# Kernel tuning notes

Hardware: AMD Instinct MI355X
Metric: run time of the kernel (lower is better)

## Reference

```python
import jax, jax.numpy as jnp
import numpy as np

B, T, S, D = 16, 64, 256, 512
NEG_INF = -1e9  # finite stand-in for -inf mask fill (identical sparsemax output, autodiff-safe)


def sparsemax(z, axis=-1):
    # sparsemax(z) = clip(z - tau, 0), tau from sorted cumsum threshold
    z = z - jnp.max(z, axis=axis, keepdims=True)
    z_srt = -jnp.sort(-z, axis=axis)                      # descending sort
    z_cum = jnp.cumsum(z_srt, axis=axis) - 1.0
    k = jnp.arange(1, z.shape[axis] + 1, dtype=z.dtype)   # rho = 1..d
    support = (k * z_srt) > z_cum
    supp_size = jnp.sum(support, axis=axis, keepdims=True)
    tau = jnp.take_along_axis(z_cum, supp_size - 1, axis=axis) / supp_size.astype(z.dtype)
    return jnp.clip(z - tau, 0.0)


def setup_inputs() -> dict:
    key = jax.random.key(0)
    ks = jax.random.split(key, 9)
    init = lambda k, shape: (jax.random.normal(k, shape, jnp.float32) * 0.05)
    return {
        "source": jax.random.normal(ks[0], (B, T, D), jnp.float32),
        "memory_bank": jax.random.normal(ks[1], (B, S, D), jnp.float32),
        "memory_mask": jax.random.randint(ks[2], (B, S), 0, 2).astype(jnp.int32),
        "W_q": init(ks[3], (D, D)),   # linear_query weight
        "b_q": init(ks[4], (D,)),     # linear_query bias
        "W_c": init(ks[5], (D, D)),   # linear_context weight (no bias)
        "v": init(ks[6], (D,)),       # v projection (dim -> 1)
        "W_out": init(ks[7], (D, 2 * D)),  # linear_out weight
        "b_out": init(ks[8], (D,)),        # linear_out bias (mlp path has bias)
    }


def reference(source, memory_bank, memory_mask, W_q, b_q, W_c, v, W_out, b_out):
    # MLP (Bahdanau) score: v^T tanh(W_q q + U_c h)
    wq = jnp.einsum('btd,ed->bte', source, W_q) + b_q        # (B,T,D)
    uh = jnp.einsum('bsd,ed->bse', memory_bank, W_c)         # (B,S,D)
    wquh = jnp.tanh(wq[:, :, None, :] + uh[:, None, :, :])   # (B,T,S,D) big intermediate
    align = jnp.einsum('btsd,d->bts', wquh, v)               # (B,T,S)
    align = jnp.where(memory_mask[:, None, :].astype(bool), align, NEG_INF)
    align_vectors = sparsemax(align, axis=-1)                # (B,T,S)
    c = jnp.einsum('bts,bsd->btd', align_vectors, memory_bank)
    concat_c = jnp.concatenate([c, source], axis=-1)         # (B,T,2D)
    attn_h = jnp.einsum('btf,df->btd', concat_c, W_out) + b_out  # no tanh on mlp path
    return attn_h.transpose(1, 0, 2), align_vectors.transpose(1, 0, 2)
```

## Files before the change

### kernel.cpp

```cpp
#include <hip/hip_runtime.h>
#include <hip/hip_bf16.h>

#define BB 16
#define TT 64
#define SS 256
#define DD 512

typedef __bf16 bf16x8 __attribute__((ext_vector_type(8)));
typedef float f32x4 __attribute__((ext_vector_type(4)));

__device__ __forceinline__ ushort f2b(float x) {
    __hip_bfloat16 h = __float2bfloat16(x);
    return __builtin_bit_cast(ushort, h);
}
__device__ __forceinline__ float b2f(ushort u) {
    unsigned int x = (unsigned int)u << 16;
    return __builtin_bit_cast(float, x);
}
__device__ __forceinline__ void gload16(const ushort* g, ushort* l) {
    __builtin_amdgcn_global_load_lds(
        (const __attribute__((address_space(1))) unsigned int*)g,
        (__attribute__((address_space(3))) unsigned int*)l, 16, 0, 0);
}

#define S_SRC (BB * TT * DD)
#define S_MB  (BB * SS * DD)
#define S_WQ  (DD * DD)
#define S_WC  (DD * DD)
#define S_WO  (DD * 2 * DD)

__global__ __launch_bounds__(256) void cast_all(
    const float* __restrict__ src, const float* __restrict__ mb,
    const float* __restrict__ wq, const float* __restrict__ wc,
    const float* __restrict__ wo,
    ushort* __restrict__ src_b, ushort* __restrict__ mb_b,
    ushort* __restrict__ wq_b, ushort* __restrict__ wc_b,
    ushort* __restrict__ wo_b) {
    int g = blockIdx.x * 256 + threadIdx.x;
    const int G0 = S_SRC / 4, G1 = S_MB / 4, G2 = S_WQ / 4, G3 = S_WC / 4;
    const float* in;
    ushort* out;
    int local;
    if (g < G0) { in = src; out = src_b; local = g; }
    else if (g < G0 + G1) { in = mb; out = mb_b; local = g - G0; }
    else if (g < G0 + G1 + G2) { in = wq; out = wq_b; local = g - G0 - G1; }
    else if (g < G0 + G1 + G2 + G3) { in = wc; out = wc_b; local = g - G0 - G1 - G2; }
    else { in = wo; out = wo_b; local = g - G0 - G1 - G2 - G3; }
    float4 x = *(const float4*)(in + (size_t)local * 4);
    ushort4 y = {f2b(x.x), f2b(x.y), f2b(x.z), f2b(x.w)};
    *(ushort4*)(out + (size_t)local * 4) = y;
}

__global__ __launch_bounds__(256) void mega_gemm(
    const ushort* __restrict__ src_b, const ushort* __restrict__ mb_b,
    const ushort* __restrict__ wq_b, const ushort* __restrict__ wc_b,
    const ushort* __restrict__ wo_b,
    const float* __restrict__ b_q, const float* __restrict__ b_out,
    float* __restrict__ Ewq, float* __restrict__ Y,
    ushort* __restrict__ Eu, ushort* __restrict__ M2) {
    __shared__ ushort Asm[64 * 64];
    __shared__ ushort Bsm[64 * 64];
    const int id = blockIdx.x;
    const ushort* Ab;
    const ushort* Bb;
    const float* bias = nullptr;
    void* Cp;
    int ldb, N, m0, n0;
    bool exp2x, obf16, hasb;
    size_t coff = 0;
    if (id < 256) {
        const bool isY = id >= 128;
        const int l = id & 127;
        m0 = (l >> 3) * 64; n0 = (l & 7) * 64;
        Ab = src_b;
        Bb = isY ? (wo_b + DD) : wq_b;
        ldb = isY ? 2 * DD : DD;
        bias = isY ? b_out : b_q;
        hasb = true; exp2x = !isY; obf16 = false; N = DD;
        Cp = isY ? (void*)Y : (void*)Ewq;
    } else if (id < 768) {
        const int l = id - 256;
        const int bz = l >> 5, tl = l & 31;
        m0 = (tl >> 3) * 64; n0 = (tl & 7) * 64;
        Ab = mb_b + (size_t)bz * SS * DD;
        Bb = wc_b;
        ldb = DD;
        hasb = false; exp2x = true; obf16 = true; N = DD;
        Cp = (void*)Eu; coff = (size_t)bz * SS * DD;
    } else {
        const int l = id - 768;
        const int bz = l >> 5, tl = l & 31;
        m0 = (tl >> 3) * 64; n0 = (tl & 7) * 64;
        Ab = mb_b + (size_t)bz * SS * DD;
        Bb = wo_b;
        ldb = 2 * DD;
        hasb = false; exp2x = false; obf16 = true; N = DD;
        Cp = (void*)M2; coff = (size_t)bz * SS * DD;
    }

    const int tid = threadIdx.x;
    const int lane = tid & 63;
    const int wave = tid >> 6;
    const int wm = wave & 1, wn = wave >> 1;

    const int rl = lane >> 3;
    const int csw = (lane & 7) ^ rl;
    const ushort* Ag0 = Ab + (size_t)(m0 + wave * 16 + rl) * DD + csw * 8;
    const ushort* Ag1 = Ag0 + (size_t)8 * DD;
    const ushort* Bg0 = Bb + (size_t)(n0 + wave * 16 + rl) * ldb + csw * 8;
    const ushort* Bg1 = Bg0 + (size_t)8 * ldb;
    ushort* Al0 = &Asm[(wave * 16) * 64];
    ushort* Al1 = &Asm[(wave * 16 + 8) * 64];
    ushort* Bl0 = &Bsm[(wave * 16) * 64];
    ushort* Bl1 = &Bsm[(wave * 16 + 8) * 64];

    const int l15 = lane & 15, quad = lane >> 4;
    const int xr = l15 & 7;
    const int arow0 = (wm * 32 + l15) * 64, arow1 = arow0 + 16 * 64;
    const int brow0 = (wn * 32 + l15) * 64, brow1 = brow0 + 16 * 64;
    const int c0 = (quad ^ xr) * 8;
    const int c1 = ((4 + quad) ^ xr) * 8;

    f32x4 acc00 = {0.f, 0.f, 0.f, 0.f}, acc01 = {0.f, 0.f, 0.f, 0.f};
    f32x4 acc10 = {0.f, 0.f, 0.f, 0.f}, acc11 = {0.f, 0.f, 0.f, 0.f};

    const int P = DD >> 6;
    for (int p = 0; p < P; ++p) {
        const int ko = p << 6;
        __syncthreads();
        gload16(Ag0 + ko, Al0);
        gload16(Ag1 + ko, Al1);
        gload16(Bg0 + ko, Bl0);
        gload16(Bg1 + ko, Bl1);
        __syncthreads();
        bf16x8 fa0 = *(const bf16x8*)&Asm[arow0 + c0];
        bf16x8 fa1 = *(const bf16x8*)&Asm[arow1 + c0];
        bf16x8 fb0 = *(const bf16x8*)&Bsm[brow0 + c0];
        bf16x8 fb1 = *(const bf16x8*)&Bsm[brow1 + c0];
        acc00 = __builtin_amdgcn_mfma_f32_16x16x32_bf16(fa0, fb0, acc00, 0, 0, 0);
        acc01 = __builtin_amdgcn_mfma_f32_16x16x32_bf16(fa0, fb1, acc01, 0, 0, 0);
        acc10 = __builtin_amdgcn_mfma_f32_16x16x32_bf16(fa1, fb0, acc10, 0, 0, 0);
        acc11 = __builtin_amdgcn_mfma_f32_16x16x32_bf16(fa1, fb1, acc11, 0, 0, 0);
        fa0 = *(const bf16x8*)&Asm[arow0 + c1];
        fa1 = *(const bf16x8*)&Asm[arow1 + c1];
        fb0 = *(const bf16x8*)&Bsm[brow0 + c1];
        fb1 = *(const bf16x8*)&Bsm[brow1 + c1];
        acc00 = __builtin_amdgcn_mfma_f32_16x16x32_bf16(fa0, fb0, acc00, 0, 0, 0);
        acc01 = __builtin_amdgcn_mfma_f32_16x16x32_bf16(fa0, fb1, acc01, 0, 0, 0);
        acc10 = __builtin_amdgcn_mfma_f32_16x16x32_bf16(fa1, fb0, acc10, 0, 0, 0);
        acc11 = __builtin_amdgcn_mfma_f32_16x16x32_bf16(fa1, fb1, acc11, 0, 0, 0);
    }
    const int nA = n0 + wn * 32 + l15;
    float bias0 = 0.f, bias1 = 0.f;
    if (hasb) { bias0 = bias[nA]; bias1 = bias[nA + 16]; }
    float* Cf = (float*)Cp;
    ushort* Cb = (ushort*)Cp;
#pragma unroll
    for (int mt = 0; mt < 2; ++mt) {
        f32x4 accN0 = mt ? acc10 : acc00;
        f32x4 accN1 = mt ? acc11 : acc01;
#pragma unroll
        for (int r = 0; r < 4; ++r) {
            int m = m0 + wm * 32 + mt * 16 + quad * 4 + r;
            float v0 = accN0[r] + bias0;
            float v1 = accN1[r] + bias1;
            if (exp2x) { v0 = __expf(2.0f * v0); v1 = __expf(2.0f * v1); }
            size_t i0 = coff + (size_t)m * N + nA;
            if (obf16) { Cb[i0] = f2b(v0); Cb[i0 + 16] = f2b(v1); }
            else { Cf[i0] = v0; Cf[i0 + 16] = v1; }
        }
    }
}

__global__ __launch_bounds__(256) void align5(const float* __restrict__ Ewq,
                                              const ushort* __restrict__ Eu,
                                              const int* __restrict__ mask,
                                              const float* __restrict__ v,
                                              const ushort* __restrict__ M2,
                                              const float* __restrict__ Y,
                                              float* __restrict__ align_out,
                                              float* __restrict__ out0) {
    const int tg = blockIdx.x, b = blockIdx.y;
    const int t0 = tg * 2, t1 = t0 + 1;
    const int bt0 = b * TT + t0, bt1 = bt0 + 1;
    const int tid = threadIdx.x;
    const int lane = tid & 63;
    const int wave = tid >> 6;
    __shared__ float4 EL[DD];
    __shared__ float zs0[SS], zs1[SS];
    __shared__ float svp[4];
    __shared__ float4 cmb[2][128];
    __shared__ int lst0[SS], lst1[SS];
    __shared__ int cnt[2];

    if (tid < 2) cnt[tid] = 0;
    const float* E0p = Ewq + (size_t)bt0 * DD;
    const float* E1p = Ewq + (size_t)bt1 * DD;
    float pv = 0.f;
    for (int d = tid; d < DD; d += 256) {
        float vv = v[d];
        EL[d] = make_float4(E0p[d], E1p[d], vv, 0.f);
        pv += vv;
    }
#pragma unroll
    for (int off = 32; off > 0; off >>= 1) pv += __shfl_xor(pv, off, 64);
    if (lane == 0) svp[wave] = pv;
    __syncthreads();
    const float sv = svp[0] + svp[1] + svp[2] + svp[3];

    const ushort* U = Eu + ((size_t)b * SS + tid) * DD;
    float a0 = 0.f, a1 = 0.f;
#pragma unroll 4
    for (int d0 = 0; d0 < DD; d0 += 8) {
        union { uint4 q; unsigned w[4]; } uw;
        uw.q = *(const uint4*)(U + d0);
#pragma unroll
        for (int jj = 0; jj < 4; ++jj) {
            unsigned wd = uw.w[jj];
            float ulo = __builtin_bit_cast(float, wd << 16);
            float uhi = __builtin_bit_cast(float, wd & 0xffff0000u);
            float4 e0 = EL[d0 + jj * 2];
            float4 e1 = EL[d0 + jj * 2 + 1];
            a0 = __builtin_fmaf(e0.z, __builtin_amdgcn_rcpf(__builtin_fmaf(e0.x, ulo, 1.0f)), a0);
            a1 = __builtin_fmaf(e0.z, __builtin_amdgcn_rcpf(__builtin_fmaf(e0.y, ulo, 1.0f)), a1);
            a0 = __builtin_fmaf(e1.z, __builtin_amdgcn_rcpf(__builtin_fmaf(e1.x, uhi, 1.0f)), a0);
            a1 = __builtin_fmaf(e1.z, __builtin_amdgcn_rcpf(__builtin_fmaf(e1.y, uhi, 1.0f)), a1);
        }
    }
    int mk = mask[b * SS + tid];
    zs0[tid] = mk ? (sv - 2.0f * a0) : -1e9f;
    zs1[tid] = mk ? (sv - 2.0f * a1) : -1e9f;
    __syncthreads();

    if (wave < 2) {
        float* zz = wave ? zs1 : zs0;
        float z0 = zz[lane];
        float z1 = zz[lane + 64];
        float z2 = zz[lane + 128];
        float z3 = zz[lane + 192];
        float mx = fmaxf(fmaxf(z0, z1), fmaxf(z2, z3));
#pragma unroll
        for (int off = 32; off > 0; off >>= 1) mx = fmaxf(mx, __shfl_xor(mx, off, 64));
        z0 -= mx; z1 -= mx; z2 -= mx; z3 -= mx;
        float lo = -1.0f, hi = 0.0f;
        for (int it = 0; it < 20; ++it) {
            float mid = 0.5f * (lo + hi);
            float ssum = fmaxf(z0 - mid, 0.f) + fmaxf(z1 - mid, 0.f) +
                         fmaxf(z2 - mid, 0.f) + fmaxf(z3 - mid, 0.f);
#pragma unroll
            for (int off = 32; off > 0; off >>= 1) ssum += __shfl_xor(ssum, off, 64);
            if (ssum >= 1.0f) lo = mid; else hi = mid;
        }
        float tau = 0.5f * (lo + hi);
        zz[lane] = fmaxf(z0 - tau, 0.f);
        zz[lane + 64] = fmaxf(z1 - tau, 0.f);
        zz[lane + 128] = fmaxf(z2 - tau, 0.f);
        zz[lane + 192] = fmaxf(z3 - tau, 0.f);
    }
    __syncthreads();

    align_out[((size_t)t0 * BB + b) * SS + tid] = zs0[tid];
    align_out[((size_t)t1 * BB + b) * SS + tid] = zs1[tid];

    if (zs0[tid] > 0.f) lst0[atomicAdd(&cnt[0], 1)] = tid;
    if (zs1[tid] > 0.f) lst1[atomicAdd(&cnt[1], 1)] = tid;
    __syncthreads();
    const int n0c = cnt[0], n1c = cnt[1];

    const int ch = tid & 127, sg = tid >> 7;
    const ushort* M2b = M2 + (size_t)b * SS * DD + ch * 4;
    float4 at0 = {0.f, 0.f, 0.f, 0.f}, at1 = {0.f, 0.f, 0.f, 0.f};
#pragma unroll 4
    for (int j = sg; j < n0c; j += 2) {
        int s = lst0[j];
        float p = zs0[s];
        ushort4 m4 = *(const ushort4*)(M2b + (size_t)s * DD);
        at0.x = __builtin_fmaf(p, b2f(m4.x), at0.x);
        at0.y = __builtin_fmaf(p, b2f(m4.y), at0.y);
        at0.z = __builtin_fmaf(p, b2f(m4.z), at0.z);
        at0.w = __builtin_fmaf(p, b2f(m4.w), at0.w);
    }
#pragma unroll 4
    for (int j = sg; j < n1c; j += 2) {
        int s = lst1[j];
        float p = zs1[s];
        ushort4 m4 = *(const ushort4*)(M2b + (size_t)s * DD);
        at1.x = __builtin_fmaf(p, b2f(m4.x), at1.x);
        at1.y = __builtin_fmaf(p, b2f(m4.y), at1.y);
        at1.z = __builtin_fmaf(p, b2f(m4.z), at1.z);
        at1.w = __builtin_fmaf(p, b2f(m4.w), at1.w);
    }
    if (sg == 1) { cmb[0][ch] = at0; cmb[1][ch] = at1; }
    __syncthreads();
    if (sg == 0) {
        float4 p0 = cmb[0][ch], p1 = cmb[1][ch];
        const float4* Y0 = (const float4*)(Y + (size_t)bt0 * DD);
        const float4* Y1 = (const float4*)(Y + (size_t)bt1 * DD);
        float4 y0 = Y0[ch], y1 = Y1[ch];
        float4 o0, o1;
        o0.x = at0.x + p0.x + y0.x; o0.y = at0.y + p0.y + y0.y;
        o0.z = at0.z + p0.z + y0.z; o0.w = at0.w + p0.w + y0.w;
        o1.x = at1.x + p1.x + y1.x; o1.y = at1.y + p1.y + y1.y;
        o1.z = at1.z + p1.z + y1.z; o1.w = at1.w + p1.w + y1.w;
        float4* O0 = (float4*)(out0 + ((size_t)t0 * BB + b) * DD);
        float4* O1 = (float4*)(out0 + ((size_t)t1 * BB + b) * DD);
        O0[ch] = o0;
        O1[ch] = o1;
    }
}

extern "C" void kernel_launch(void* const* d_in, const int* in_sizes, int n_in,
                              void* d_out, int out_size, void* d_ws, size_t ws_size,
                              hipStream_t stream) {
    const float* source = (const float*)d_in[0];
    const float* memory_bank = (const float*)d_in[1];
    const int* memory_mask = (const int*)d_in[2];
    const float* W_q = (const float*)d_in[3];
    const float* b_q = (const float*)d_in[4];
    const float* W_c = (const float*)d_in[5];
    const float* v = (const float*)d_in[6];
    const float* W_out = (const float*)d_in[7];
    const float* b_out = (const float*)d_in[8];

    float* out0 = (float*)d_out;
    float* out1 = out0 + (size_t)TT * BB * DD;

    float* Ewq = (float*)d_ws;
    float* Y = Ewq + S_SRC;
    ushort* Eu = (ushort*)(Y + S_SRC);
    ushort* M2 = Eu + S_MB;
    ushort* src_b = M2 + S_MB;
    ushort* mb_b = src_b + S_SRC;
    ushort* wqw_b = mb_b + S_MB;
    ushort* wcw_b = wqw_b + S_WQ;
    ushort* wo_b = wcw_b + S_WC;

    dim3 blk(256);
    int ngroups = (S_SRC + S_MB + S_WQ + S_WC + S_WO) / 4;
    cast_all<<<dim3(ngroups / 256), blk, 0, stream>>>(
        source, memory_bank, W_q, W_c, W_out, src_b, mb_b, wqw_b, wcw_b, wo_b);
    mega_gemm<<<dim3(1280), blk, 0, stream>>>(
        src_b, mb_b, wqw_b, wcw_b, wo_b, b_q, b_out, Ewq, Y, Eu, M2);
    align5<<<dim3(TT / 2, BB), blk, 0, stream>>>(
        Ewq, Eu, memory_mask, v, M2, Y, out1, out0);
}
```

Baseline: 123.0 us.

## Compact unmasked positions and pair reciprocals in alignment score loop

The alignment kernel now builds a compacted list of unmasked memory positions using a ballot and prefix count, and computes tanh scores only for those, splitting the D dimension across two half-block groups. Masked positions always get zero sparsemax weight, so their score work can be dropped. The inner loop also merges two reciprocal calls into one by combining fractions, which trades an rcp for extra multiplies and carries some overflow or precision risk. An all-masked fallback path outputs uniform weights.

```diff
diff --git a/kernel.cpp b/kernel.cpp
--- a/kernel.cpp
+++ b/kernel.cpp
@@ -172,7 +172,7 @@
     }
 }
 
-__global__ __launch_bounds__(256) void align5(const float* __restrict__ Ewq,
+__global__ __launch_bounds__(256) void align6(const float* __restrict__ Ewq,
                                               const ushort* __restrict__ Eu,
                                               const int* __restrict__ mask,
                                               const float* __restrict__ v,
@@ -187,13 +187,21 @@
     const int lane = tid & 63;
     const int wave = tid >> 6;
     __shared__ float4 EL[DD];
-    __shared__ float zs0[SS], zs1[SS];
+    __shared__ float pa[2][2][SS];
+    __shared__ float zc0[SS], zc1[SS];
+    __shared__ float pf0[SS], pf1[SS];
+    __shared__ int lst[SS];
+    __shared__ int lstS0[SS], lstS1[SS];
+    __shared__ float4 cmb[2][128];
     __shared__ float svp[4];
-    __shared__ float4 cmb[2][128];
-    __shared__ int lst0[SS], lst1[SS];
+    __shared__ int wcnt[4];
     __shared__ int cnt[2];
 
     if (tid < 2) cnt[tid] = 0;
+    const int mk = mask[b * SS + tid];
+    const unsigned long long bal = __ballot(mk != 0);
+    const int wr = __popcll(bal & ((1ull << lane) - 1ull));
+    if (lane == 0) wcnt[wave] = __popcll(bal);
     const float* E0p = Ewq + (size_t)bt0 * DD;
     const float* E1p = Ewq + (size_t)bt1 * DD;
     float pv = 0.f;
@@ -202,42 +210,88 @@
         EL[d] = make_float4(E0p[d], E1p[d], vv, 0.f);
         pv += vv;
     }
+    pf0[tid] = 0.f;
+    pf1[tid] = 0.f;
 #pragma unroll
     for (int off = 32; off > 0; off >>= 1) pv += __shfl_xor(pv, off, 64);
     if (lane == 0) svp[wave] = pv;
     __syncthreads();
     const float sv = svp[0] + svp[1] + svp[2] + svp[3];
-
-    const ushort* U = Eu + ((size_t)b * SS + tid) * DD;
-    float a0 = 0.f, a1 = 0.f;
+    int base = 0;
+    for (int w = 0; w < wave; ++w) base += wcnt[w];
+    const int na = wcnt[0] + wcnt[1] + wcnt[2] + wcnt[3];
+    if (mk) lst[base + wr] = tid;
+    __syncthreads();
+
+    if (na == 0) {
+        const float u = 1.0f / (float)SS;
+        align_out[((size_t)t0 * BB + b) * SS + tid] = u;
+        align_out[((size_t)t1 * BB + b) * SS + tid] = u;
+        const int ch = tid & 127, sg = tid >> 7;
+        if (sg == 0) {
+            const ushort* M2b = M2 + (size_t)b * SS * DD + ch * 4;
+            float4 at = {0.f, 0.f, 0.f, 0.f};
+            for (int s = 0; s < SS; ++s) {
+                ushort4 m4 = *(const ushort4*)(M2b + (size_t)s * DD);
+                at.x += b2f(m4.x); at.y += b2f(m4.y);
+                at.z += b2f(m4.z); at.w += b2f(m4.w);
+            }
+            const float4* Y0 = (const float4*)(Y + (size_t)bt0 * DD);
+            const float4* Y1 = (const float4*)(Y + (size_t)bt1 * DD);
+            float4 y0 = Y0[ch], y1 = Y1[ch];
+            float4 o0 = {at.x * u + y0.x, at.y * u + y0.y, at.z * u + y0.z, at.w * u + y0.w};
+            float4 o1 = {at.x * u + y1.x, at.y * u + y1.y, at.z * u + y1.z, at.w * u + y1.w};
+            ((float4*)(out0 + ((size_t)t0 * BB + b) * DD))[ch] = o0;
+            ((float4*)(out0 + ((size_t)t1 * BB + b) * DD))[ch] = o1;
+        }
+        return;
+    }
+
+    const int ci0 = tid & 127, dh = tid >> 7;
+    const int dbase = dh * 256;
+    for (int ci = ci0; ci < na; ci += 128) {
+        const int s = lst[ci];
+        const ushort* U = Eu + ((size_t)b * SS + s) * DD + dbase;
+        float a0 = 0.f, a1 = 0.f;
 #pragma unroll 4
-    for (int d0 = 0; d0 < DD; d0 += 8) {
-        union { uint4 q; unsigned w[4]; } uw;
-        uw.q = *(const uint4*)(U + d0);
-#pragma unroll
-        for (int jj = 0; jj < 4; ++jj) {
-            unsigned wd = uw.w[jj];
-            float ulo = __builtin_bit_cast(float, wd << 16);
-            float uhi = __builtin_bit_cast(float, wd & 0xffff0000u);
-            float4 e0 = EL[d0 + jj * 2];
-            float4 e1 = EL[d0 + jj * 2 + 1];
-            a0 = __builtin_fmaf(e0.z, __builtin_amdgcn_rcpf(__builtin_fmaf(e0.x, ulo, 1.0f)), a0);
-            a1 = __builtin_fmaf(e0.z, __builtin_amdgcn_rcpf(__builtin_fmaf(e0.y, ulo, 1.0f)), a1);
-            a0 = __builtin_fmaf(e1.z, __builtin_amdgcn_rcpf(__builtin_fmaf(e1.x, uhi, 1.0f)), a0);
-            a1 = __builtin_fmaf(e1.z, __builtin_amdgcn_rcpf(__builtin_fmaf(e1.y, uhi, 1.0f)), a1);
+        for (int dd = 0; dd < 256; dd += 8) {
+            union { uint4 q; unsigned w[4]; } uw;
+            uw.q = *(const uint4*)(U + dd);
+#pragma unroll
+            for (int jj = 0; jj < 4; ++jj) {
+                const unsigned wd = uw.w[jj];
+                const float ulo = __builtin_bit_cast(float, wd << 16);
+                const float uhi = __builtin_bit_cast(float, wd & 0xffff0000u);
+                const float4 eA = EL[dbase + dd + jj * 2];
+                const float4 eB = EL[dbase + dd + jj * 2 + 1];
+                const float d0 = __builtin_fmaf(eA.x, ulo, 1.0f);
+                const float d1 = __builtin_fmaf(eB.x, uhi, 1.0f);
+                float num = eA.z * d1;
+                num = __builtin_fmaf(eB.z, d0, num);
+                a0 = __builtin_fmaf(num, __builtin_amdgcn_rcpf(d0 * d1), a0);
+                const float e0 = __builtin_fmaf(eA.y, ulo, 1.0f);
+                const float e1 = __builtin_fmaf(eB.y, uhi, 1.0f);
+                float nu1 = eA.z * e1;
+                nu1 = __builtin_fmaf(eB.z, e0, nu1);
+                a1 = __builtin_fmaf(nu1, __builtin_amdgcn_rcpf(e0 * e1), a1);
+            }
         }
-    }
-    int mk = mask[b * SS + tid];
-    zs0[tid] = mk ? (sv - 2.0f * a0) : -1e9f;
-    zs1[tid] = mk ? (sv - 2.0f * a1) : -1e9f;
+        pa[dh][0][ci] = a0;
+        pa[dh][1][ci] = a1;
+    }
+    __syncthreads();
+    for (int ci = tid; ci < na; ci += 256) {
+        zc0[ci] = sv - 2.0f * (pa[0][0][ci] + pa[1][0][ci]);
+        zc1[ci] = sv - 2.0f * (pa[0][1][ci] + pa[1][1][ci]);
+    }
     __syncthreads();
 
     if (wave < 2) {
-        float* zz = wave ? zs1 : zs0;
-        float z0 = zz[lane];
-        float z1 = zz[lane + 64];
-        float z2 = zz[lane + 128];
-        float z3 = zz[lane + 192];
+        float* zz = wave ? zc1 : zc0;
+        float z0 = lane < na ? zz[lane] : -1e9f;
+        float z1 = lane + 64 < na ? zz[lane + 64] : -1e9f;
+        float z2 = lane + 128 < na ? zz[lane + 128] : -1e9f;
+        float z3 = lane + 192 < na ? zz[lane + 192] : -1e9f;
         float mx = fmaxf(fmaxf(z0, z1), fmaxf(z2, z3));
 #pragma unroll
         for (int off = 32; off > 0; off >>= 1) mx = fmaxf(mx, __shfl_xor(mx, off, 64));
@@ -252,19 +306,24 @@
             if (ssum >= 1.0f) lo = mid; else hi = mid;
         }
         float tau = 0.5f * (lo + hi);
-        zz[lane] = fmaxf(z0 - tau, 0.f);
-        zz[lane + 64] = fmaxf(z1 - tau, 0.f);
-        zz[lane + 128] = fmaxf(z2 - tau, 0.f);
-        zz[lane + 192] = fmaxf(z3 - tau, 0.f);
-    }
-    __syncthreads();
-
-    align_out[((size_t)t0 * BB + b) * SS + tid] = zs0[tid];
-    align_out[((size_t)t1 * BB + b) * SS + tid] = zs1[tid];
-
-    if (zs0[tid] > 0.f) lst0[atomicAdd(&cnt[0], 1)] = tid;
-    if (zs1[tid] > 0.f) lst1[atomicAdd(&cnt[1], 1)] = tid;
-    __syncthreads();
+        if (lane < na) zz[lane] = fmaxf(z0 - tau, 0.f);
+        if (lane + 64 < na) zz[lane + 64] = fmaxf(z1 - tau, 0.f);
+        if (lane + 128 < na) zz[lane + 128] = fmaxf(z2 - tau, 0.f);
+        if (lane + 192 < na) zz[lane + 192] = fmaxf(z3 - tau, 0.f);
+    }
+    __syncthreads();
+
+    for (int ci = tid; ci < na; ci += 256) {
+        const int s = lst[ci];
+        const float p0 = zc0[ci], p1 = zc1[ci];
+        pf0[s] = p0;
+        pf1[s] = p1;
+        if (p0 > 0.f) lstS0[atomicAdd(&cnt[0], 1)] = s;
+        if (p1 > 0.f) lstS1[atomicAdd(&cnt[1], 1)] = s;
+    }
+    __syncthreads();
+    align_out[((size_t)t0 * BB + b) * SS + tid] = pf0[tid];
+    align_out[((size_t)t1 * BB + b) * SS + tid] = pf1[tid];
     const int n0c = cnt[0], n1c = cnt[1];
 
     const int ch = tid & 127, sg = tid >> 7;
@@ -272,8 +331,8 @@
     float4 at0 = {0.f, 0.f, 0.f, 0.f}, at1 = {0.f, 0.f, 0.f, 0.f};
 #pragma unroll 4
     for (int j = sg; j < n0c; j += 2) {
-        int s = lst0[j];
-        float p = zs0[s];
+        int s = lstS0[j];
+        float p = pf0[s];
         ushort4 m4 = *(const ushort4*)(M2b + (size_t)s * DD);
         at0.x = __builtin_fmaf(p, b2f(m4.x), at0.x);
         at0.y = __builtin_fmaf(p, b2f(m4.y), at0.y);
@@ -282,8 +341,8 @@
     }
 #pragma unroll 4
     for (int j = sg; j < n1c; j += 2) {
-        int s = lst1[j];
-        float p = zs1[s];
+        int s = lstS1[j];
+        float p = pf1[s];
         ushort4 m4 = *(const ushort4*)(M2b + (size_t)s * DD);
         at1.x = __builtin_fmaf(p, b2f(m4.x), at1.x);
         at1.y = __builtin_fmaf(p, b2f(m4.y), at1.y);
@@ -341,6 +400,6 @@
         source, memory_bank, W_q, W_c, W_out, src_b, mb_b, wqw_b, wcw_b, wo_b);
     mega_gemm<<<dim3(1280), blk, 0, stream>>>(
         src_b, mb_b, wqw_b, wcw_b, wo_b, b_q, b_out, Ewq, Y, Eu, M2);
-    align5<<<dim3(TT / 2, BB), blk, 0, stream>>>(
+    align6<<<dim3(TT / 2, BB), blk, 0, stream>>>(
         Ewq, Eu, memory_mask, v, M2, Y, out1, out0);
 }
```

Result: no change. 120.8 us (median of 2 runs) (-1.8%).
